# Optimization experiments

Measured on AMD Instinct MI355X. Metric: run time of the kernel, lower is better.

Reference implementation:

```python
import math
import jax, jax.numpy as jnp
import numpy as np

N, H, E, K = 8192, 2048, 8, 2
CF = 1.25


def setup_inputs() -> dict:
    key = jax.random.key(0)
    ks = jax.random.split(key, 5)
    s1 = 1.0 / math.sqrt(H)
    s2 = 1.0 / math.sqrt(2 * H)
    return {
        "tokens": jax.random.normal(ks[0], (N, H), jnp.float32),
        "Wr": jax.random.normal(ks[1], (E, H), jnp.float32) * s1,   # router: logits = x @ Wr.T + br
        "br": jnp.zeros((E,), jnp.float32),
        "W1": jax.random.normal(ks[2], (E, H, 2 * H), jnp.float32) * s1,
        "b1": jnp.zeros((E, 2 * H), jnp.float32),
        "W2": jax.random.normal(ks[3], (E, 2 * H, H), jnp.float32) * s2,
        "b2": jnp.zeros((E, H), jnp.float32),
    }


def reference(tokens, Wr, br, W1, b1, W2, b2):
    n = tokens.shape[0]
    cap = max(1, math.ceil(CF * n / E))  # per-expert capacity (static)

    # --- router + top-k ---
    logits = tokens @ Wr.T + br                         # [N, E]
    scores, expert_ids = jax.lax.top_k(logits, K)       # [N, K]
    probs = jax.nn.softmax(scores, axis=-1)

    # --- flatten dispatches and sort by expert (stable, like the torch code) ---
    flat_e = expert_ids.reshape(-1)                     # [N*K]
    flat_t = jnp.repeat(jnp.arange(n), K)               # [N*K]
    flat_s = probs.reshape(-1).astype(tokens.dtype)     # [N*K]
    order = jnp.argsort(flat_e)                         # jnp.argsort is stable
    se, st, ss = flat_e[order], flat_t[order], flat_s[order]

    # --- capacity-limited gather: fixed [E, cap] index grid ---
    seg_start = jnp.searchsorted(se, jnp.arange(E))     # [E] first slot of each expert segment
    counts = jnp.bincount(se, length=E)                 # [E] tokens routed to each expert
    slot = jnp.arange(cap)
    idx = jnp.clip(seg_start[:, None] + slot[None, :], 0, n * K - 1)  # [E, cap]
    valid = slot[None, :] < jnp.minimum(counts, cap)[:, None]          # [E, cap]
    tok_idx = st[idx]                                   # [E, cap] source token ids
    w = jnp.where(valid, ss[idx], 0.0)[..., None]       # [E, cap, 1] combine weights (0 => dropped)

    # --- grouped per-expert FFN (GEMM over [E, cap, H]) ---
    x = tokens[tok_idx]                                 # [E, cap, H]
    h = jax.nn.gelu(jnp.einsum('ech,ehf->ecf', x, W1) + b1[:, None, :], approximate=False)
    y = jnp.einsum('ecf,efh->ech', h, W2) + b2[:, None, :]

    # --- weighted scatter-add combine ---
    out = jnp.zeros_like(tokens).at[tok_idx.reshape(-1)].add((y * w).reshape(-1, tokens.shape[-1]))
    return out
```

## Files before the change

### kernel.cpp

```cpp
#include <hip/hip_runtime.h>
#include <hip/hip_bf16.h>
#include <math.h>

#define NTOK 8192
#define HDIM 2048
#define NEXP 8
#define TOPK 2
#define CAP  1280
#define FF   4096
#define BK   32

typedef float  f32x4  __attribute__((ext_vector_type(4)));
typedef __bf16 bf16x8 __attribute__((ext_vector_type(8)));

typedef __attribute__((address_space(1))) const unsigned int gas_u32;
typedef __attribute__((address_space(3))) unsigned int las_u32;

__device__ __forceinline__ void gload16(const void* g, void* l) {
    __builtin_amdgcn_global_load_lds((gas_u32*)g, (las_u32*)l, 16, 0, 0);
}

__device__ __forceinline__ ushort f2bf(float f) {
    union { float f; unsigned u; } c; c.f = f;
    unsigned u = c.u;
    unsigned r = (u + 0x7FFFu + ((u >> 16) & 1u)) >> 16;
    return (ushort)r;
}
__device__ __forceinline__ float bf2f(ushort h) {
    union { unsigned u; float f; } c; c.u = ((unsigned)h) << 16;
    return c.f;
}

__global__ void k_convert(const float* __restrict__ src, ushort* __restrict__ dst) {
    int i = (blockIdx.x * 256 + threadIdx.x) * 8;
    float4 a = *(const float4*)(src + i);
    float4 b = *(const float4*)(src + i + 4);
    uint4 o;
    o.x = (unsigned)f2bf(a.x) | ((unsigned)f2bf(a.y) << 16);
    o.y = (unsigned)f2bf(a.z) | ((unsigned)f2bf(a.w) << 16);
    o.z = (unsigned)f2bf(b.x) | ((unsigned)f2bf(b.y) << 16);
    o.w = (unsigned)f2bf(b.z) | ((unsigned)f2bf(b.w) << 16);
    *(uint4*)(dst + i) = o;
}

__global__ void k_router(const float* __restrict__ tokens, const float* __restrict__ Wr,
                         const float* __restrict__ br, int* __restrict__ eids,
                         float* __restrict__ probs) {
    int wave = threadIdx.x >> 6, lane = threadIdx.x & 63;
    int t = blockIdx.x * 4 + wave;
    const float* tp = tokens + (size_t)t * HDIM;
    double acc[NEXP];
    #pragma unroll
    for (int e = 0; e < NEXP; ++e) acc[e] = 0.0;
    for (int j = 0; j < HDIM / 64; ++j) {
        float x = tp[j * 64 + lane];
        #pragma unroll
        for (int e = 0; e < NEXP; ++e)
            acc[e] += (double)x * (double)Wr[e * HDIM + j * 64 + lane];
    }
    #pragma unroll
    for (int e = 0; e < NEXP; ++e) {
        #pragma unroll
        for (int off = 32; off; off >>= 1) acc[e] += __shfl_xor(acc[e], off, 64);
    }
    if (lane == 0) {
        float lg[NEXP];
        #pragma unroll
        for (int e = 0; e < NEXP; ++e) lg[e] = (float)acc[e] + br[e];
        int e0 = 0; float s0 = lg[0];
        #pragma unroll
        for (int e = 1; e < NEXP; ++e) if (lg[e] > s0) { s0 = lg[e]; e0 = e; }
        int e1 = -1; float s1 = -1e30f;
        #pragma unroll
        for (int e = 0; e < NEXP; ++e) if (e != e0 && lg[e] > s1) { s1 = lg[e]; e1 = e; }
        float ex = expf(s1 - s0);
        float den = 1.f + ex;
        eids[t * 2] = e0; eids[t * 2 + 1] = e1;
        probs[t * 2] = 1.f / den; probs[t * 2 + 1] = ex / den;
    }
}

__global__ void k_assign(const int* __restrict__ eids, int* __restrict__ tok_map,
                         int* __restrict__ dest) {
    __shared__ int cnt[64][NEXP];
    int l = threadIdx.x;
    for (int i = l; i < NEXP * CAP; i += 64) tok_map[i] = 0;
    int c[NEXP];
    #pragma unroll
    for (int e = 0; e < NEXP; ++e) c[e] = 0;
    const int base = l * 256;
    for (int i = 0; i < 256; ++i) {
        int ee = eids[base + i];
        #pragma unroll
        for (int e = 0; e < NEXP; ++e) c[e] += (ee == e);
    }
    #pragma unroll
    for (int e = 0; e < NEXP; ++e) cnt[l][e] = c[e];
    __syncthreads();
    if (l < NEXP) {
        int run = 0;
        for (int b = 0; b < 64; ++b) { int v = cnt[b][l]; cnt[b][l] = run; run += v; }
    }
    __syncthreads();
    int off[NEXP];
    #pragma unroll
    for (int e = 0; e < NEXP; ++e) off[e] = cnt[l][e];
    for (int i = 0; i < 256; ++i) {
        int d = base + i;
        int ee = eids[d];
        int r = -1;
        #pragma unroll
        for (int e = 0; e < NEXP; ++e) { bool m = (ee == e); if (m) r = off[e]; off[e] += m; }
        if (r < CAP) { tok_map[ee * CAP + r] = d >> 1; dest[d] = ee * CAP + r; }
        else dest[d] = -1;
    }
}

__global__ __launch_bounds__(256) void k_transpose(const float* __restrict__ src,
                                                   ushort* __restrict__ dst,
                                                   int Kd, int Nd) {
    __shared__ float tl[64][65];
    int e = blockIdx.z;
    int k0 = blockIdx.x * 64, n0 = blockIdx.y * 64;
    const float* s = src + (size_t)e * Kd * Nd;
    ushort* d = dst + (size_t)e * Kd * Nd;
    int tid = threadIdx.x;
    #pragma unroll
    for (int i = 0; i < 4; ++i) {
        int flat = (i * 256 + tid) * 4;
        int kk = flat >> 6, nn = flat & 63;
        float4 v = *(const float4*)(s + (size_t)(k0 + kk) * Nd + n0 + nn);
        tl[kk][nn] = v.x; tl[kk][nn + 1] = v.y; tl[kk][nn + 2] = v.z; tl[kk][nn + 3] = v.w;
    }
    __syncthreads();
    #pragma unroll
    for (int g = 0; g < 4; ++g) {
        int flat = g * 1024 + tid * 4;
        int nn = flat >> 6, kk = flat & 63;
        uint2 o;
        o.x = (unsigned)f2bf(tl[kk][nn])     | ((unsigned)f2bf(tl[kk + 1][nn]) << 16);
        o.y = (unsigned)f2bf(tl[kk + 2][nn]) | ((unsigned)f2bf(tl[kk + 3][nn]) << 16);
        *(uint2*)(d + (size_t)(n0 + nn) * Kd + k0 + kk) = o;
    }
}

#define SCHED0() __builtin_amdgcn_sched_barrier(0)
#define VMC4()   do { asm volatile("s_waitcnt vmcnt(4)" ::: "memory"); } while (0)

template<bool DOGELU, bool GATHER>
__global__ __launch_bounds__(256) void k_gemm(const ushort* __restrict__ A,
                                              const int* __restrict__ tmap,
                                              const ushort* __restrict__ B,
                                              const float* __restrict__ bias,
                                              ushort* __restrict__ C,
                                              int Kd, int Nd) {
    __shared__ __attribute__((aligned(128))) char lds[49152];
    const int tid  = threadIdx.x;
    const int lane = tid & 63;
    const int wave = tid >> 6;
    const int wr = wave >> 1, wc = wave & 1;
    const int e = blockIdx.z;
    const int bm0 = blockIdx.y * 128, bn0 = blockIdx.x * 128;

    const ushort* Be = B + (size_t)e * (size_t)Nd * Kd;
    const int R  = tid >> 2;
    const int kc = (tid & 3) * 8;
    int ra0, ra1;
    if (GATHER) { ra0 = tmap[e * CAP + bm0 + R]; ra1 = tmap[e * CAP + bm0 + R + 64]; }
    else        { ra0 = e * CAP + bm0 + R;       ra1 = e * CAP + bm0 + R + 64; }
    const ushort* pa0 = A + (size_t)ra0 * Kd + kc;
    const ushort* pa1 = A + (size_t)ra1 * Kd + kc;
    const ushort* pb0 = Be + (size_t)(bn0 + R) * Kd + kc;
    const ushort* pb1 = Be + (size_t)(bn0 + R + 64) * Kd + kc;
    const int ldsW = wave * 1024;

    auto STAGE = [&](int buf, int kt) {
        char* d = lds + buf * 16384;
        gload16(pa0 + kt * BK, d + ldsW);
        gload16(pa1 + kt * BK, d + 4096 + ldsW);
        gload16(pb0 + kt * BK, d + 8192 + ldsW);
        gload16(pb1 + kt * BK, d + 12288 + ldsW);
    };

    const int fr = lane & 15, kq = lane >> 4;
    const int cb = kq * 16;
    int offA[4], offB[4];
    #pragma unroll
    for (int mi = 0; mi < 4; ++mi) offA[mi] = (wr * 64 + mi * 16 + fr) * 64 + cb;
    #pragma unroll
    for (int ni = 0; ni < 4; ++ni) offB[ni] = 8192 + (wc * 64 + ni * 16 + fr) * 64 + cb;

    f32x4 acc[4][4] = {};
    const int nt = Kd / BK;

    STAGE(0, 0); STAGE(1, 1);
    for (int t = 0; t < nt; ++t) {
        VMC4();
        __builtin_amdgcn_s_barrier();
        SCHED0();
        STAGE((t + 2) % 3, min(t + 2, nt - 1));
        const char* rb = lds + (t % 3) * 16384;
        bf16x8 af[4], bf[4];
        #pragma unroll
        for (int mi = 0; mi < 4; ++mi) af[mi] = *(const bf16x8*)(rb + offA[mi]);
        #pragma unroll
        for (int ni = 0; ni < 4; ++ni) bf[ni] = *(const bf16x8*)(rb + offB[ni]);
        #pragma unroll
        for (int mi = 0; mi < 4; ++mi)
            #pragma unroll
            for (int ni = 0; ni < 4; ++ni)
                acc[mi][ni] = __builtin_amdgcn_mfma_f32_16x16x32_bf16(af[mi], bf[ni],
                                                                      acc[mi][ni], 0, 0, 0);
    }

    const float* be = bias + e * Nd;
    ushort* Ce = C + (size_t)e * CAP * Nd;
    const int rl = (lane >> 4) * 4, cl = lane & 15;
    #pragma unroll
    for (int mi = 0; mi < 4; ++mi) {
        #pragma unroll
        for (int ni = 0; ni < 4; ++ni) {
            #pragma unroll
            for (int r = 0; r < 4; ++r) {
                int gr = bm0 + wr * 64 + mi * 16 + rl + r;
                int gc = bn0 + wc * 64 + ni * 16 + cl;
                float v = acc[mi][ni][r] + be[gc];
                if (DOGELU) v = 0.5f * v * (1.f + erff(v * 0.70710678118654752f));
                Ce[(size_t)gr * Nd + gc] = f2bf(v);
            }
        }
    }
}

__global__ void k_combine(const ushort* __restrict__ Y, const int* __restrict__ dest,
                          const float* __restrict__ probs, float* __restrict__ out) {
    int t = blockIdx.x;
    int h0 = threadIdx.x * 8;
    int d0 = dest[t * 2], d1 = dest[t * 2 + 1];
    float p0 = d0 >= 0 ? probs[t * 2] : 0.f;
    float p1 = d1 >= 0 ? probs[t * 2 + 1] : 0.f;
    int r0 = d0 >= 0 ? d0 : 0, r1 = d1 >= 0 ? d1 : 0;
    uint4 a = *(const uint4*)(Y + (size_t)r0 * HDIM + h0);
    uint4 b = *(const uint4*)(Y + (size_t)r1 * HDIM + h0);
    float4 o0, o1;
    o0.x = p0 * bf2f(a.x & 0xffff) + p1 * bf2f(b.x & 0xffff);
    o0.y = p0 * bf2f(a.x >> 16)    + p1 * bf2f(b.x >> 16);
    o0.z = p0 * bf2f(a.y & 0xffff) + p1 * bf2f(b.y & 0xffff);
    o0.w = p0 * bf2f(a.y >> 16)    + p1 * bf2f(b.y >> 16);
    o1.x = p0 * bf2f(a.z & 0xffff) + p1 * bf2f(b.z & 0xffff);
    o1.y = p0 * bf2f(a.z >> 16)    + p1 * bf2f(b.z >> 16);
    o1.z = p0 * bf2f(a.w & 0xffff) + p1 * bf2f(b.w & 0xffff);
    o1.w = p0 * bf2f(a.w >> 16)    + p1 * bf2f(b.w >> 16);
    float* op = out + (size_t)t * HDIM + h0;
    *(float4*)op = o0;
    *(float4*)(op + 4) = o1;
}

extern "C" void kernel_launch(void* const* d_in, const int* in_sizes, int n_in,
                              void* d_out, int out_size, void* d_ws, size_t ws_size,
                              hipStream_t stream) {
    const float* tokens = (const float*)d_in[0];
    const float* Wr     = (const float*)d_in[1];
    const float* br     = (const float*)d_in[2];
    const float* W1     = (const float*)d_in[3];
    const float* b1     = (const float*)d_in[4];
    const float* W2     = (const float*)d_in[5];
    const float* b2     = (const float*)d_in[6];
    float* out = (float*)d_out;
    char* ws = (char*)d_ws;

    int*    eids    = (int*)(ws);
    float*  probs   = (float*)(ws + 65536);
    int*    tok_map = (int*)(ws + 131072);
    int*    dest    = (int*)(ws + 172032);
    size_t off = 1u << 20;
    ushort* TbY = (ushort*)(ws + off);
    off += 41943040;
    ushort* Hm  = (ushort*)(ws + off);
    off += 83886080;
    ushort* WT  = (ushort*)(ws + off);
    (void)in_sizes; (void)n_in; (void)out_size; (void)ws_size;

    k_convert<<<dim3(NTOK * HDIM / 2048), 256, 0, stream>>>(tokens, TbY);
    k_router<<<dim3(NTOK / 4), 256, 0, stream>>>(tokens, Wr, br, eids, probs);
    k_assign<<<dim3(1), 64, 0, stream>>>(eids, tok_map, dest);
    k_transpose<<<dim3(HDIM / 64, FF / 64, NEXP), 256, 0, stream>>>(W1, WT, HDIM, FF);
    k_gemm<true, true><<<dim3(FF / 128, CAP / 128, NEXP), 256, 0, stream>>>(
        TbY, tok_map, WT, b1, Hm, HDIM, FF);
    k_transpose<<<dim3(FF / 64, HDIM / 64, NEXP), 256, 0, stream>>>(W2, WT, FF, HDIM);
    k_gemm<false, false><<<dim3(HDIM / 128, CAP / 128, NEXP), 256, 0, stream>>>(
        Hm, nullptr, WT, b2, TbY, FF, HDIM);
    k_combine<<<dim3(NTOK), 256, 0, stream>>>(TbY, dest, probs, out);
}
```

Before: 738.0 us.

## Double K tile to 64 with XOR-swizzled LDS and double buffering

```diff
diff --git a/kernel.cpp b/kernel.cpp
--- a/kernel.cpp
+++ b/kernel.cpp
@@ -8,7 +8,7 @@
 #define TOPK 2
 #define CAP  1280
 #define FF   4096
-#define BK   32
+#define BK   64
 
 typedef float  f32x4  __attribute__((ext_vector_type(4)));
 typedef __bf16 bf16x8 __attribute__((ext_vector_type(8)));
@@ -145,7 +145,7 @@
 }
 
 #define SCHED0() __builtin_amdgcn_sched_barrier(0)
-#define VMC4()   do { asm volatile("s_waitcnt vmcnt(4)" ::: "memory"); } while (0)
+#define VMC0()   do { asm volatile("s_waitcnt vmcnt(0)" ::: "memory"); } while (0)
 
 template<bool DOGELU, bool GATHER>
 __global__ __launch_bounds__(256) void k_gemm(const ushort* __restrict__ A,
@@ -154,7 +154,7 @@
                                               const float* __restrict__ bias,
                                               ushort* __restrict__ C,
                                               int Kd, int Nd) {
-    __shared__ __attribute__((aligned(128))) char lds[49152];
+    __shared__ __attribute__((aligned(128))) char lds[65536];
     const int tid  = threadIdx.x;
     const int lane = tid & 63;
     const int wave = tid >> 6;
@@ -163,54 +163,75 @@
     const int bm0 = blockIdx.y * 128, bn0 = blockIdx.x * 128;
 
     const ushort* Be = B + (size_t)e * (size_t)Nd * Kd;
-    const int R  = tid >> 2;
-    const int kc = (tid & 3) * 8;
-    int ra0, ra1;
-    if (GATHER) { ra0 = tmap[e * CAP + bm0 + R]; ra1 = tmap[e * CAP + bm0 + R + 64]; }
-    else        { ra0 = e * CAP + bm0 + R;       ra1 = e * CAP + bm0 + R + 64; }
-    const ushort* pa0 = A + (size_t)ra0 * Kd + kc;
-    const ushort* pa1 = A + (size_t)ra1 * Kd + kc;
-    const ushort* pb0 = Be + (size_t)(bn0 + R) * Kd + kc;
-    const ushort* pb1 = Be + (size_t)(bn0 + R + 64) * Kd + kc;
-    const int ldsW = wave * 1024;
+    const int rbase = tid >> 3;
+    const int kc = (((tid & 7) ^ (rbase & 7))) * 8;
+    const ushort* pa[4]; const ushort* pb[4];
+    #pragma unroll
+    for (int r = 0; r < 4; ++r) {
+        int gr = r * 32 + rbase;
+        int arow = GATHER ? tmap[e * CAP + bm0 + gr] : (e * CAP + bm0 + gr);
+        pa[r] = A  + (size_t)arow * Kd + kc;
+        pb[r] = Be + (size_t)(bn0 + gr) * Kd + kc;
+    }
 
     auto STAGE = [&](int buf, int kt) {
-        char* d = lds + buf * 16384;
-        gload16(pa0 + kt * BK, d + ldsW);
-        gload16(pa1 + kt * BK, d + 4096 + ldsW);
-        gload16(pb0 + kt * BK, d + 8192 + ldsW);
-        gload16(pb1 + kt * BK, d + 12288 + ldsW);
+        char* d = lds + buf * 32768;
+        #pragma unroll
+        for (int r = 0; r < 4; ++r)
+            gload16(pa[r] + kt * BK, d + r * 4096 + tid * 16);
+        #pragma unroll
+        for (int r = 0; r < 4; ++r)
+            gload16(pb[r] + kt * BK, d + 16384 + r * 4096 + tid * 16);
     };
 
     const int fr = lane & 15, kq = lane >> 4;
-    const int cb = kq * 16;
-    int offA[4], offB[4];
-    #pragma unroll
-    for (int mi = 0; mi < 4; ++mi) offA[mi] = (wr * 64 + mi * 16 + fr) * 64 + cb;
-    #pragma unroll
-    for (int ni = 0; ni < 4; ++ni) offB[ni] = 8192 + (wc * 64 + ni * 16 + fr) * 64 + cb;
+    int offA[4][2], offB[4][2];
+    #pragma unroll
+    for (int m = 0; m < 4; ++m) {
+        int row = wr * 64 + m * 16 + fr;
+        #pragma unroll
+        for (int ks = 0; ks < 2; ++ks)
+            offA[m][ks] = row * 128 + (((ks * 4 + kq) ^ (row & 7)) * 16);
+    }
+    #pragma unroll
+    for (int n = 0; n < 4; ++n) {
+        int row = wc * 64 + n * 16 + fr;
+        #pragma unroll
+        for (int ks = 0; ks < 2; ++ks)
+            offB[n][ks] = 16384 + row * 128 + (((ks * 4 + kq) ^ (row & 7)) * 16);
+    }
 
     f32x4 acc[4][4] = {};
     const int nt = Kd / BK;
 
-    STAGE(0, 0); STAGE(1, 1);
+    STAGE(0, 0);
+    VMC0();
+    __builtin_amdgcn_s_barrier();
     for (int t = 0; t < nt; ++t) {
-        VMC4();
+        if (t + 1 < nt) STAGE((t + 1) & 1, t + 1);
+        SCHED0();
+        const char* rb = lds + (t & 1) * 32768;
+        bf16x8 af[4][2], bf[4][2];
+        #pragma unroll
+        for (int m = 0; m < 4; ++m)
+            #pragma unroll
+            for (int ks = 0; ks < 2; ++ks)
+                af[m][ks] = *(const bf16x8*)(rb + offA[m][ks]);
+        #pragma unroll
+        for (int n = 0; n < 4; ++n)
+            #pragma unroll
+            for (int ks = 0; ks < 2; ++ks)
+                bf[n][ks] = *(const bf16x8*)(rb + offB[n][ks]);
+        #pragma unroll
+        for (int ks = 0; ks < 2; ++ks)
+            #pragma unroll
+            for (int m = 0; m < 4; ++m)
+                #pragma unroll
+                for (int n = 0; n < 4; ++n)
+                    acc[m][n] = __builtin_amdgcn_mfma_f32_16x16x32_bf16(af[m][ks], bf[n][ks],
+                                                                        acc[m][n], 0, 0, 0);
+        VMC0();
         __builtin_amdgcn_s_barrier();
-        SCHED0();
-        STAGE((t + 2) % 3, min(t + 2, nt - 1));
-        const char* rb = lds + (t % 3) * 16384;
-        bf16x8 af[4], bf[4];
-        #pragma unroll
-        for (int mi = 0; mi < 4; ++mi) af[mi] = *(const bf16x8*)(rb + offA[mi]);
-        #pragma unroll
-        for (int ni = 0; ni < 4; ++ni) bf[ni] = *(const bf16x8*)(rb + offB[ni]);
-        #pragma unroll
-        for (int mi = 0; mi < 4; ++mi)
-            #pragma unroll
-            for (int ni = 0; ni < 4; ++ni)
-                acc[mi][ni] = __builtin_amdgcn_mfma_f32_16x16x32_bf16(af[mi], bf[ni],
-                                                                      acc[mi][ni], 0, 0, 0);
     }
 
     const float* be = bias + e * Nd;
```

After: 732.0 us. Within noise of the previous version (-0.8%).
